# Optimization experiments

Measured on AMD Instinct MI355X. Metric: run time of the kernel, lower is better.

## Reference

```python
import jax, jax.numpy as jnp
import numpy as np

B, C, H, W = 8, 3, 512, 512
EPS = 2e-4
N_ITER = 10  # n_iter_max default in TvChambolleDenoiser.forward


def setup_inputs() -> dict:
    key = jax.random.key(0)
    k1, k2 = jax.random.split(key)
    image = jax.random.normal(k1, (B, C, H, W), dtype=jnp.float32)
    # per-image denoising strength, typical TV weights
    weight = jax.random.uniform(k2, (B,), dtype=jnp.float32, minval=0.05, maxval=0.15)
    return {"image": image, "weight": weight}


def _denoise_tv_2d(img, w, eps=EPS, n_iter=N_ITER):
    """Chambolle TV denoising of a single 2D image (faithful to the torch loop)."""
    tau = 0.25  # 1 / (2 * ndim), ndim = 2
    numel = img.shape[0] * img.shape[1]

    def body(carry, i):
        pt, out, E_init, E_prev, done = carry
        # divergence of dual variable pt: dt = -pt.sum(0); dt[1:,:] += pt[0,:-1,:]; dt[:,1:] += pt[1,:,:-1]
        dt = -(pt[0] + pt[1])
        dt = dt.at[1:, :].add(pt[0, :-1, :])
        dt = dt.at[:, 1:].add(pt[1, :, :-1])
        out_new = jnp.where(i > 0, img + dt, img)
        Et = jnp.where(i > 0, jnp.sum(dt * dt), jnp.float32(0.0))
        # forward finite differences, zero-padded at the far boundary (gt stays 0 there)
        g0 = jnp.pad(out_new[1:, :] - out_new[:-1, :], ((0, 1), (0, 0)))
        g1 = jnp.pad(out_new[:, 1:] - out_new[:, :-1], ((0, 0), (0, 1)))
        s = g0 * g0 + g1 * g1
        # safe sqrt (forward value identical; avoids NaN grads at exact zeros)
        norm = jnp.sqrt(jnp.where(s > 0, s, 1.0)) * (s > 0)
        Et = (Et + w * jnp.sum(norm)) / numel
        gt = jnp.stack([g0, g1])  # [2, H, W]
        pt_new = (pt - tau * gt) / (1.0 + (tau / w) * norm)[None]
        E_init_new = jnp.where(i == 0, Et, E_init)
        converged = (i > 0) & (jnp.abs(E_prev - Et) < eps * E_init_new)
        # once converged (break in the torch loop), freeze all state
        pt = jnp.where(done, pt, pt_new)
        out = jnp.where(done, out, out_new)
        E_prev = jnp.where(done, E_prev, Et)
        E_init = jnp.where(done, E_init, E_init_new)
        done = done | converged
        return (pt, out, E_init, E_prev, done), None

    carry0 = (
        jnp.zeros((2,) + img.shape, img.dtype),  # pt
        img,                                      # out
        jnp.float32(0.0),                         # E_init
        jnp.float32(0.0),                         # E_previous
        jnp.bool_(False),                         # done
    )
    (pt, out, E_init, E_prev, done), _ = jax.lax.scan(body, carry0, jnp.arange(n_iter))
    return out


def reference(image, weight):
    b, c, h, w = image.shape
    imgs = image.reshape(b * c, h, w)          # each (batch, channel) slice denoised independently
    ws = jnp.repeat(weight, c)                 # per-batch weight shared across channels
    out = jax.vmap(_denoise_tv_2d)(imgs, ws)
    return out.reshape(b, c, h, w)
```

## Files before the change

kernel.cpp:

```cpp
#include <hip/hip_runtime.h>
#include <hip/hip_fp16.h>
#include <math.h>
#include <stdint.h>

#define HH 512
#define WW 512
#define NIMG 24
#define CCH 3
#define TAU 0.25f
#define TVEPS 2e-4f
#define NUMEL 262144.0f

#define LSF 69
#define LSH 70


__device__ __forceinline__ float2 h2f(uint32_t v) {
    __half2 h; *reinterpret_cast<uint32_t*>(&h) = v;
    return __half22float2(h);
}
__device__ __forceinline__ uint32_t f2h2(float a, float b) {
    __half2 h = __floats2half2_rn(a, b);
    return *reinterpret_cast<uint32_t*>(&h);
}
__device__ __forceinline__ void h4_to_f(uint2 hv, float* f) {
    float2 a = h2f(hv.x), b = h2f(hv.y);
    f[0] = a.x; f[1] = a.y; f[2] = b.x; f[3] = b.y;
}

struct Smem {
    uint32_t PT[68 * LSF];
    float    OA[68 * LSF];
    __half   IM[68 * LSH];
};

__device__ __forceinline__ int SUMIX(int slot, int arr, int im) {
    return ((slot * 4 + arr) * NIMG + im) * 64;
}

__device__ void stage_pt_im(Smem& S, const uint32_t* __restrict__ ptg,
                            const __half* __restrict__ hI,
                            int x0, int y0, int tid) {
    for (int idx = tid; idx < 68 * 34; idx += 256) {
        int r = idx / 34, mq = idx - r * 34;
        int c = 2 * mq;
        int y = y0 - 2 + r, x = x0 - 2 + c;
        uint2 pv = make_uint2(0u, 0u);
        uint32_t iv = 0u;
        if ((unsigned)y < (unsigned)HH && (unsigned)x < (unsigned)WW) {
            size_t off = (size_t)y * WW + x;
            pv = *(const uint2*)(ptg + off);
            iv = *(const uint32_t*)(hI + off);
        }
        S.PT[r * LSF + c] = pv.x;
        S.PT[r * LSF + c + 1] = pv.y;
        *(uint32_t*)&S.IM[r * LSH + c] = iv;
    }
}

template <bool ACC>
__device__ float phase_outA(Smem& S, int tid) {
    float acc = 0.f;
    for (int idx = tid; idx < 67 * 67; idx += 256) {
        int r = idx / 67, c = idx - r * 67;
        r += 1; c += 1;
        float2 cf = h2f(S.PT[r * LSF + c]);
        float up = h2f(S.PT[(r - 1) * LSF + c]).x;
        float lf = h2f(S.PT[r * LSF + c - 1]).y;
        float im = __half2float(S.IM[r * LSH + c]);
        float oa = im + (-(cf.x + cf.y) + up + lf);
        S.OA[r * LSF + c] = oa;
        if (ACC) {
            if (r >= 2 && r < 66 && c >= 2 && c < 66) {
                float d = oa - im;
                acc += d * d;
            }
        }
    }
    return acc;
}

template <bool ACC>
__device__ float phase_ptA(Smem& S, int x0, int y0, int tid, float tw) {
    float acc = 0.f;
    for (int idx = tid; idx < 66 * 66; idx += 256) {
        int r = idx / 66, c = idx - r * 66;
        r += 1; c += 1;
        int y = y0 - 2 + r, x = x0 - 2 + c;
        if ((unsigned)y < (unsigned)HH && (unsigned)x < (unsigned)WW) {
            float o = S.OA[r * LSF + c];
            float g0 = (y < HH - 1) ? S.OA[(r + 1) * LSF + c] - o : 0.f;
            float g1 = (x < WW - 1) ? S.OA[r * LSF + c + 1] - o : 0.f;
            float ss2 = g0 * g0 + g1 * g1;
            float nrm = (ss2 > 0.f) ? sqrtf(ss2) : 0.f;
            if (ACC) {
                if (r >= 2 && r < 66 && c >= 2 && c < 66) acc += nrm;
            }
            float inv = __builtin_amdgcn_rcpf(1.f + tw * nrm);
            float2 cf = h2f(S.PT[r * LSF + c]);
            S.PT[r * LSF + c] = f2h2((cf.x - TAU * g0) * inv, (cf.y - TAU * g1) * inv);
        } else {
            S.PT[r * LSF + c] = 0u;
        }
    }
    return acc;
}

template <bool ACC>
__device__ float phase_outB(Smem& S, int tid) {
    float acc = 0.f;
    for (int idx = tid; idx < 65 * 65; idx += 256) {
        int r = idx / 65, c = idx - r * 65;
        r += 2; c += 2;
        float2 cf = h2f(S.PT[r * LSF + c]);
        float im = __half2float(S.IM[r * LSH + c]);
        float ob = im + (-(cf.x + cf.y) + h2f(S.PT[(r - 1) * LSF + c]).x
                         + h2f(S.PT[r * LSF + c - 1]).y);
        S.OA[r * LSF + c] = ob;
        if (ACC) {
            if (r < 66 && c < 66) {
                float d = ob - im;
                acc += d * d;
            }
        }
    }
    return acc;
}

__device__ float phase_ptB_store(Smem& S, uint32_t* __restrict__ poutI,
                                 int x0, int y0, int tid, float tw) {
    const int tx = tid & 15, ry = tid >> 4;
    const int gxb = x0 + 4 * tx;
    float acc = 0.f;
    #pragma unroll
    for (int i = 0; i < 4; ++i) {
        int gy = y0 + ry + 16 * i;
        int r = 2 + ry + 16 * i;
        uint32_t pv[4];
        #pragma unroll
        for (int j = 0; j < 4; ++j) {
            int c = 2 + 4 * tx + j;
            float o = S.OA[r * LSF + c];
            float g0 = (gy < HH - 1) ? S.OA[(r + 1) * LSF + c] - o : 0.f;
            float g1 = (gxb + j < WW - 1) ? S.OA[r * LSF + c + 1] - o : 0.f;
            float ss2 = g0 * g0 + g1 * g1;
            float nrm = (ss2 > 0.f) ? sqrtf(ss2) : 0.f;
            acc += nrm;
            float inv = __builtin_amdgcn_rcpf(1.f + tw * nrm);
            float2 cf = h2f(S.PT[r * LSF + c]);
            pv[j] = f2h2((cf.x - TAU * g0) * inv, (cf.y - TAU * g1) * inv);
        }
        *(uint4*)(poutI + (size_t)gy * WW + gxb) = make_uint4(pv[0], pv[1], pv[2], pv[3]);
    }
    return acc;
}

__device__ __forceinline__ void red4_store(float a, float b, float c, float d,
                                           float* pa, float* pb, float* pc, float* pdd,
                                           int tid) {
    for (int off = 32; off > 0; off >>= 1) {
        a += __shfl_down(a, off, 64);
        b += __shfl_down(b, off, 64);
        c += __shfl_down(c, off, 64);
        d += __shfl_down(d, off, 64);
    }
    __shared__ float sr[4][4];
    int wave = tid >> 6, lane = tid & 63;
    if (lane == 0) { sr[0][wave] = a; sr[1][wave] = b; sr[2][wave] = c; sr[3][wave] = d; }
    __syncthreads();
    if (tid == 0) {
        *pa = (sr[0][0] + sr[0][1]) + (sr[0][2] + sr[0][3]);
        *pb = (sr[1][0] + sr[1][1]) + (sr[1][2] + sr[1][3]);
        *pc = (sr[2][0] + sr[2][1]) + (sr[2][2] + sr[2][3]);
        *pdd = (sr[3][0] + sr[3][1]) + (sr[3][2] + sr[3][3]);
    }
}

__global__ __launch_bounds__(256, 4) void tv_step0(
    const float* __restrict__ img, const float* __restrict__ weight,
    __half* __restrict__ imgh, uint32_t* __restrict__ ptout,
    float* __restrict__ pn0)
{
    const int im = blockIdx.z;
    const int bid = blockIdx.y * 8 + blockIdx.x;
    const float w = weight[im / CCH];
    const int x0 = blockIdx.x * 64, y0 = blockIdx.y * 64;
    const float* imgI = img + (size_t)im * HH * WW;
    __half* hI = imgh + (size_t)im * HH * WW;
    uint32_t* pI = ptout + (size_t)im * HH * WW;
    __shared__ float s[65][68];
    const int tid = threadIdx.x;
    const int tx = tid & 15, ry = tid >> 4;
    const int gx = x0 + 4 * tx;

    float o[4][4];
    #pragma unroll
    for (int i = 0; i < 4; ++i) {
        int ey = ry + 16 * i, gy = y0 + ey;
        float4 v = *(const float4*)(imgI + (size_t)gy * WW + gx);
        o[i][0] = v.x; o[i][1] = v.y; o[i][2] = v.z; o[i][3] = v.w;
        *(float4*)&s[ey][4 * tx] = v;
    }
    if (tx == 15 && x0 + 64 < WW) {
        #pragma unroll
        for (int i = 0; i < 4; ++i) {
            int ey = ry + 16 * i, gy = y0 + ey;
            s[ey][64] = imgI[(size_t)gy * WW + x0 + 64];
        }
    }
    if (ry == 0 && y0 + 64 < HH) {
        *(float4*)&s[64][4 * tx] = *(const float4*)(imgI + (size_t)(y0 + 64) * WW + gx);
    }
    __syncthreads();

    float accn = 0.f;
    const float tw = TAU / w;
    #pragma unroll
    for (int i = 0; i < 4; ++i) {
        int ey = ry + 16 * i, gy = y0 + ey;
        float4 dn = *(float4*)&s[ey + 1][4 * tx];
        float rt_sh = __shfl_down(o[i][0], 1, 64);
        float rt = (tx == 15) ? s[ey][64] : rt_sh;
        float dnv[4] = {dn.x, dn.y, dn.z, dn.w};
        uint32_t pv[4];
        #pragma unroll
        for (int j = 0; j < 4; ++j) {
            float ov = o[i][j];
            float g0 = (gy < HH - 1) ? dnv[j] - ov : 0.f;
            float rn = (j < 3) ? o[i][j + 1] : rt;
            float g1 = (gx + j < WW - 1) ? rn - ov : 0.f;
            float ss2 = g0 * g0 + g1 * g1;
            float nrm = (ss2 > 0.f) ? sqrtf(ss2) : 0.f;
            accn += nrm;
            float inv = __builtin_amdgcn_rcpf(1.f + tw * nrm);
            pv[j] = f2h2(-TAU * g0 * inv, -TAU * g1 * inv);
        }
        size_t off = (size_t)gy * WW + gx;
        *(uint4*)(pI + off) = make_uint4(pv[0], pv[1], pv[2], pv[3]);
        *(uint2*)(hI + off) = make_uint2(f2h2(o[i][0], o[i][1]), f2h2(o[i][2], o[i][3]));
    }
    for (int off = 32; off > 0; off >>= 1) accn += __shfl_down(accn, off, 64);
    __shared__ float sr[4];
    if ((tid & 63) == 0) sr[tid >> 6] = accn;
    __syncthreads();
    if (tid == 0) pn0[im * 64 + bid] = (sr[0] + sr[1]) + (sr[2] + sr[3]);
}

__global__ __launch_bounds__(256, 3) void tv_fused(
    int m,
    const __half* __restrict__ imgh, const float* __restrict__ weight,
    const uint32_t* __restrict__ pt_in, uint32_t* __restrict__ pt_out,
    float* __restrict__ sc, float* __restrict__ sums)
{
    const int im = blockIdx.z;
    const int bid = blockIdx.y * 8 + blockIdx.x;
    const int tid = threadIdx.x;
    const float w = weight[im / CCH];

    __shared__ int sh_done;
    {
        const int sIn = (m - 1) & 1;
        if (tid < 64) {
            float da = 0.f, na = 0.f, db = 0.f, nb = 0.f;
            if (m == 1) {
                na = sums[SUMIX(0, 1, im) + tid];
            } else {
                da = sums[SUMIX(sIn, 0, im) + tid];
                na = sums[SUMIX(sIn, 1, im) + tid];
                db = sums[SUMIX(sIn, 2, im) + tid];
                nb = sums[SUMIX(sIn, 3, im) + tid];
            }
            for (int off = 32; off > 0; off >>= 1) {
                da += __shfl_down(da, off, 64);
                na += __shfl_down(na, off, 64);
                db += __shfl_down(db, off, 64);
                nb += __shfl_down(nb, off, 64);
            }
            if (tid == 0) {
                float Eprev, Einit; int done, lastk;
                if (m == 1) {
                    float E0 = w * na / NUMEL;
                    Eprev = E0; Einit = E0; done = 0; lastk = 0;
                } else {
                    const float* sI = sc + sIn * 128;
                    Eprev = sI[im]; Einit = sI[32 + im];
                    done = ((const int*)sI)[64 + im];
                    lastk = ((const int*)sI)[96 + im];
                    if (!done) {
                        float Et = (da + w * na) / NUMEL;
                        if (fabsf(Eprev - Et) < TVEPS * Einit) { done = 1; lastk = 2 * m - 3; }
                        else {
                            Eprev = Et;
                            Et = (db + w * nb) / NUMEL;
                            if (fabsf(Eprev - Et) < TVEPS * Einit) { done = 1; lastk = 2 * m - 2; }
                            else Eprev = Et;
                        }
                    }
                }
                if (bid == 0) {
                    float* sO = sc + (m & 1) * 128;
                    sO[im] = Eprev; sO[32 + im] = Einit;
                    ((int*)sO)[64 + im] = done;
                    ((int*)sO)[96 + im] = lastk;
                }
                sh_done = done;
            }
        }
    }
    __syncthreads();
    if (sh_done) return;

    const int x0 = blockIdx.x * 64, y0 = blockIdx.y * 64;
    const float tw = TAU / w;
    const uint32_t* pinI = pt_in + (size_t)im * HH * WW;
    uint32_t* poutI = pt_out + (size_t)im * HH * WW;
    const __half* hI = imgh + (size_t)im * HH * WW;

    __shared__ Smem S;
    stage_pt_im(S, pinI, hI, x0, y0, tid);
    __syncthreads();
    float a_d = phase_outA<true>(S, tid);
    __syncthreads();
    float a_n = phase_ptA<true>(S, x0, y0, tid, tw);
    __syncthreads();
    float b_d = phase_outB<true>(S, tid);
    __syncthreads();
    float b_n = phase_ptB_store(S, poutI, x0, y0, tid, tw);

    const int sOut = m & 1;
    red4_store(a_d, a_n, b_d, b_n,
               &sums[SUMIX(sOut, 0, im) + bid], &sums[SUMIX(sOut, 1, im) + bid],
               &sums[SUMIX(sOut, 2, im) + bid], &sums[SUMIX(sOut, 3, im) + bid], tid);
}

__global__ __launch_bounds__(256, 3) void tv_out(
    const float* __restrict__ img, float* __restrict__ out,
    const uint32_t* __restrict__ ptA, const uint32_t* __restrict__ ptB,
    const __half* __restrict__ imgh, const float* __restrict__ weight,
    const float* __restrict__ sc, const float* __restrict__ sums)
{
    const int im = blockIdx.z;
    const int tid = threadIdx.x;
    const float w = weight[im / CCH];

    __shared__ int2 shk;
    {
        const float* sI = sc;
        int done = ((const int*)sI)[64 + im];
        int lastk = ((const int*)sI)[96 + im];
        if (!done && tid < 64) {
            float da = sums[SUMIX(0, 0, im) + tid];
            float na = sums[SUMIX(0, 1, im) + tid];
            float db = sums[SUMIX(0, 2, im) + tid];
            float nb = sums[SUMIX(0, 3, im) + tid];
            for (int off = 32; off > 0; off >>= 1) {
                da += __shfl_down(da, off, 64);
                na += __shfl_down(na, off, 64);
                db += __shfl_down(db, off, 64);
                nb += __shfl_down(nb, off, 64);
            }
            if (tid == 0) {
                float Eprev = sI[im], Einit = sI[32 + im];
                float Et = (da + w * na) / NUMEL;
                if (fabsf(Eprev - Et) < TVEPS * Einit) { done = 1; lastk = 7; }
                else {
                    Eprev = Et;
                    Et = (db + w * nb) / NUMEL;
                    if (fabsf(Eprev - Et) < TVEPS * Einit) { done = 1; lastk = 8; }
                }
            }
        }
        if (tid == 0) { shk.x = done; shk.y = lastk; }
    }
    __syncthreads();
    const int k = shk.x ? shk.y : 9;

    const float* imgI = img + (size_t)im * HH * WW;
    float* outI = out + (size_t)im * HH * WW;
    const int x0 = blockIdx.x * 64, y0 = blockIdx.y * 64;
    const int tx = tid & 15, ry = tid >> 4;
    const int gx = x0 + 4 * tx;

    if (k & 1) {
        const uint32_t* p = ((((k - 1) >> 1) & 1) ? ptB : ptA) + (size_t)im * HH * WW;
        #pragma unroll
        for (int i = 0; i < 4; ++i) {
            int gy = y0 + ry + 16 * i;
            size_t off = (size_t)gy * WW + gx;
            uint4 cv = *(const uint4*)(p + off);
            uint4 uv = make_uint4(0u, 0u, 0u, 0u);
            if (gy > 0) uv = *(const uint4*)(p + off - WW);
            uint32_t lf = (gx > 0) ? p[off - 1] : 0u;
            float4 iv = *(const float4*)(imgI + off);
            uint32_t cc[4] = {cv.x, cv.y, cv.z, cv.w};
            uint32_t uu[4] = {uv.x, uv.y, uv.z, uv.w};
            uint32_t lt[4] = {lf, cv.x, cv.y, cv.z};
            float ivv[4] = {iv.x, iv.y, iv.z, iv.w};
            float r[4];
            #pragma unroll
            for (int j = 0; j < 4; ++j) {
                float2 cf = h2f(cc[j]);
                r[j] = ivv[j] + (-(cf.x + cf.y) + h2f(uu[j]).x + h2f(lt[j]).y);
            }
            *(float4*)(outI + off) = make_float4(r[0], r[1], r[2], r[3]);
        }
    } else {
        const uint32_t* p = ((((k - 2) >> 1) & 1) ? ptB : ptA) + (size_t)im * HH * WW;
        const __half* hI = imgh + (size_t)im * HH * WW;
        const float tw = TAU / w;
        __shared__ Smem S;
        stage_pt_im(S, p, hI, x0, y0, tid);
        __syncthreads();
        phase_outA<false>(S, tid);
        __syncthreads();
        phase_ptA<false>(S, x0, y0, tid, tw);
        __syncthreads();
        #pragma unroll
        for (int i = 0; i < 4; ++i) {
            int gy = y0 + ry + 16 * i;
            int r = 2 + ry + 16 * i;
            size_t off = (size_t)gy * WW + gx;
            float4 iv = *(const float4*)(imgI + off);
            float ivv[4] = {iv.x, iv.y, iv.z, iv.w};
            float rr[4];
            #pragma unroll
            for (int j = 0; j < 4; ++j) {
                int c = 2 + 4 * tx + j;
                float2 cf = h2f(S.PT[r * LSF + c]);
                float up = h2f(S.PT[(r - 1) * LSF + c]).x;
                float lf = h2f(S.PT[r * LSF + c - 1]).y;
                rr[j] = ivv[j] + (-(cf.x + cf.y) + up + lf);
            }
            *(float4*)(outI + off) = make_float4(rr[0], rr[1], rr[2], rr[3]);
        }
    }
}

extern "C" void kernel_launch(void* const* d_in, const int* in_sizes, int n_in,
                              void* d_out, int out_size, void* d_ws, size_t ws_size,
                              hipStream_t stream)
{
    const float* img = (const float*)d_in[0];
    const float* weight = (const float*)d_in[1];
    float* out = (float*)d_out;
    float* sc = (float*)d_ws;
    float* sums = (float*)((char*)d_ws + 4096);
    __half* imgh = (__half*)((char*)d_ws + 65536);
    uint32_t* ptA = (uint32_t*)((char*)d_ws + 12648448);
    uint32_t* ptB = (uint32_t*)((char*)d_ws + 37814272);

    dim3 grid(8, 8, NIMG);
    dim3 block(256);

    tv_step0<<<grid, block, 0, stream>>>(img, weight, imgh, ptA,
                                         sums + (0 * 4 + 1) * NIMG * 64);

    for (int m = 1; m <= 4; ++m) {
        uint32_t* pin  = (m & 1) ? ptA : ptB;
        uint32_t* pout = (m & 1) ? ptB : ptA;
        tv_fused<<<grid, block, 0, stream>>>(m, imgh, weight, pin, pout, sc, sums);
    }

    tv_out<<<grid, block, 0, stream>>>(img, out, ptA, ptB, imgh, weight, sc, sums);
}
```

Measured before the change: 280.2 us.

## Keep fused two-step TV tile in registers with shuffle-based halo exchange

The fused two-iteration kernel stops staging a 68x68 halo tile through shared memory with strided per-phase loops. Each thread now holds a 4x4 register patch, exchanges horizontal neighbours with wave shuffles and vertical neighbours through small shared buffers, and recomputes the one- and two-pixel halo ring explicitly on edge threads. This cuts LDS traffic and index arithmetic, at the cost of much higher register pressure (launch bounds lowered to 2 blocks per SIMD target) and more divergent edge-thread code.

```diff
diff --git a/kernel.cpp b/kernel.cpp
--- a/kernel.cpp
+++ b/kernel.cpp
@@ -28,15 +28,36 @@
     f[0] = a.x; f[1] = a.y; f[2] = b.x; f[3] = b.y;
 }
 
+__device__ __forceinline__ int SUMIX(int slot, int arr, int im) {
+    return ((slot * 4 + arr) * NIMG + im) * 64;
+}
+
+__device__ __forceinline__ void red4_store(float a, float b, float c, float d,
+                                           float* pa, float* pb, float* pc, float* pdd,
+                                           int tid) {
+    for (int off = 32; off > 0; off >>= 1) {
+        a += __shfl_down(a, off, 64);
+        b += __shfl_down(b, off, 64);
+        c += __shfl_down(c, off, 64);
+        d += __shfl_down(d, off, 64);
+    }
+    __shared__ float sr[4][4];
+    int wave = tid >> 6, lane = tid & 63;
+    if (lane == 0) { sr[0][wave] = a; sr[1][wave] = b; sr[2][wave] = c; sr[3][wave] = d; }
+    __syncthreads();
+    if (tid == 0) {
+        *pa = (sr[0][0] + sr[0][1]) + (sr[0][2] + sr[0][3]);
+        *pb = (sr[1][0] + sr[1][1]) + (sr[1][2] + sr[1][3]);
+        *pc = (sr[2][0] + sr[2][1]) + (sr[2][2] + sr[2][3]);
+        *pdd = (sr[3][0] + sr[3][1]) + (sr[3][2] + sr[3][3]);
+    }
+}
+
 struct Smem {
     uint32_t PT[68 * LSF];
     float    OA[68 * LSF];
     __half   IM[68 * LSH];
 };
-
-__device__ __forceinline__ int SUMIX(int slot, int arr, int im) {
-    return ((slot * 4 + arr) * NIMG + im) * 64;
-}
 
 __device__ void stage_pt_im(Smem& S, const uint32_t* __restrict__ ptg,
                             const __half* __restrict__ hI,
@@ -58,9 +79,7 @@
     }
 }
 
-template <bool ACC>
-__device__ float phase_outA(Smem& S, int tid) {
-    float acc = 0.f;
+__device__ void phase_outA_x(Smem& S, int tid) {
     for (int idx = tid; idx < 67 * 67; idx += 256) {
         int r = idx / 67, c = idx - r * 67;
         r += 1; c += 1;
@@ -68,21 +87,11 @@
         float up = h2f(S.PT[(r - 1) * LSF + c]).x;
         float lf = h2f(S.PT[r * LSF + c - 1]).y;
         float im = __half2float(S.IM[r * LSH + c]);
-        float oa = im + (-(cf.x + cf.y) + up + lf);
-        S.OA[r * LSF + c] = oa;
-        if (ACC) {
-            if (r >= 2 && r < 66 && c >= 2 && c < 66) {
-                float d = oa - im;
-                acc += d * d;
-            }
-        }
-    }
-    return acc;
-}
-
-template <bool ACC>
-__device__ float phase_ptA(Smem& S, int x0, int y0, int tid, float tw) {
-    float acc = 0.f;
+        S.OA[r * LSF + c] = im + (-(cf.x + cf.y) + up + lf);
+    }
+}
+
+__device__ void phase_ptA_x(Smem& S, int x0, int y0, int tid, float tw) {
     for (int idx = tid; idx < 66 * 66; idx += 256) {
         int r = idx / 66, c = idx - r * 66;
         r += 1; c += 1;
@@ -93,86 +102,12 @@
             float g1 = (x < WW - 1) ? S.OA[r * LSF + c + 1] - o : 0.f;
             float ss2 = g0 * g0 + g1 * g1;
             float nrm = (ss2 > 0.f) ? sqrtf(ss2) : 0.f;
-            if (ACC) {
-                if (r >= 2 && r < 66 && c >= 2 && c < 66) acc += nrm;
-            }
             float inv = __builtin_amdgcn_rcpf(1.f + tw * nrm);
             float2 cf = h2f(S.PT[r * LSF + c]);
             S.PT[r * LSF + c] = f2h2((cf.x - TAU * g0) * inv, (cf.y - TAU * g1) * inv);
         } else {
             S.PT[r * LSF + c] = 0u;
         }
-    }
-    return acc;
-}
-
-template <bool ACC>
-__device__ float phase_outB(Smem& S, int tid) {
-    float acc = 0.f;
-    for (int idx = tid; idx < 65 * 65; idx += 256) {
-        int r = idx / 65, c = idx - r * 65;
-        r += 2; c += 2;
-        float2 cf = h2f(S.PT[r * LSF + c]);
-        float im = __half2float(S.IM[r * LSH + c]);
-        float ob = im + (-(cf.x + cf.y) + h2f(S.PT[(r - 1) * LSF + c]).x
-                         + h2f(S.PT[r * LSF + c - 1]).y);
-        S.OA[r * LSF + c] = ob;
-        if (ACC) {
-            if (r < 66 && c < 66) {
-                float d = ob - im;
-                acc += d * d;
-            }
-        }
-    }
-    return acc;
-}
-
-__device__ float phase_ptB_store(Smem& S, uint32_t* __restrict__ poutI,
-                                 int x0, int y0, int tid, float tw) {
-    const int tx = tid & 15, ry = tid >> 4;
-    const int gxb = x0 + 4 * tx;
-    float acc = 0.f;
-    #pragma unroll
-    for (int i = 0; i < 4; ++i) {
-        int gy = y0 + ry + 16 * i;
-        int r = 2 + ry + 16 * i;
-        uint32_t pv[4];
-        #pragma unroll
-        for (int j = 0; j < 4; ++j) {
-            int c = 2 + 4 * tx + j;
-            float o = S.OA[r * LSF + c];
-            float g0 = (gy < HH - 1) ? S.OA[(r + 1) * LSF + c] - o : 0.f;
-            float g1 = (gxb + j < WW - 1) ? S.OA[r * LSF + c + 1] - o : 0.f;
-            float ss2 = g0 * g0 + g1 * g1;
-            float nrm = (ss2 > 0.f) ? sqrtf(ss2) : 0.f;
-            acc += nrm;
-            float inv = __builtin_amdgcn_rcpf(1.f + tw * nrm);
-            float2 cf = h2f(S.PT[r * LSF + c]);
-            pv[j] = f2h2((cf.x - TAU * g0) * inv, (cf.y - TAU * g1) * inv);
-        }
-        *(uint4*)(poutI + (size_t)gy * WW + gxb) = make_uint4(pv[0], pv[1], pv[2], pv[3]);
-    }
-    return acc;
-}
-
-__device__ __forceinline__ void red4_store(float a, float b, float c, float d,
-                                           float* pa, float* pb, float* pc, float* pdd,
-                                           int tid) {
-    for (int off = 32; off > 0; off >>= 1) {
-        a += __shfl_down(a, off, 64);
-        b += __shfl_down(b, off, 64);
-        c += __shfl_down(c, off, 64);
-        d += __shfl_down(d, off, 64);
-    }
-    __shared__ float sr[4][4];
-    int wave = tid >> 6, lane = tid & 63;
-    if (lane == 0) { sr[0][wave] = a; sr[1][wave] = b; sr[2][wave] = c; sr[3][wave] = d; }
-    __syncthreads();
-    if (tid == 0) {
-        *pa = (sr[0][0] + sr[0][1]) + (sr[0][2] + sr[0][3]);
-        *pb = (sr[1][0] + sr[1][1]) + (sr[1][2] + sr[1][3]);
-        *pc = (sr[2][0] + sr[2][1]) + (sr[2][2] + sr[2][3]);
-        *pdd = (sr[3][0] + sr[3][1]) + (sr[3][2] + sr[3][3]);
     }
 }
 
@@ -246,7 +181,7 @@
     if (tid == 0) pn0[im * 64 + bid] = (sr[0] + sr[1]) + (sr[2] + sr[3]);
 }
 
-__global__ __launch_bounds__(256, 3) void tv_fused(
+__global__ __launch_bounds__(256, 2) void tv_fused(
     int m,
     const __half* __restrict__ imgh, const float* __restrict__ weight,
     const uint32_t* __restrict__ pt_in, uint32_t* __restrict__ pt_out,
@@ -316,19 +251,419 @@
     uint32_t* poutI = pt_out + (size_t)im * HH * WW;
     const __half* hI = imgh + (size_t)im * HH * WW;
 
-    __shared__ Smem S;
-    stage_pt_im(S, pinI, hI, x0, y0, tid);
+    const int tx = tid & 15, ty = tid >> 4;
+    const int gx = x0 + 4 * tx, gy0 = y0 + 4 * ty;
+    const bool hasN = y0 > 0, hasW = x0 > 0;
+    const bool hasS = y0 + 64 < HH, hasE = x0 + 64 < WW;
+
+    __shared__ uint4  XB[16][16];
+    __shared__ float4 OB[16][16];
+    __shared__ float  WO[17];
+    __shared__ float  EO[17];
+    __shared__ uint32_t EP[16];
+
+    uint4 c[4]; uint2 ih[4];
+    #pragma unroll
+    for (int i = 0; i < 4; ++i) {
+        size_t off = (size_t)(gy0 + i) * WW + gx;
+        c[i] = *(const uint4*)(pinI + off);
+        ih[i] = *(const uint2*)(hI + off);
+    }
+    XB[ty][tx] = c[3];
+
+    uint4 png0 = make_uint4(0u,0u,0u,0u), png1 = make_uint4(0u,0u,0u,0u);
+    uint2 ihN = make_uint2(0u, 0u);
+    if (ty == 0 && hasN) {
+        png0 = *(const uint4*)(pinI + (size_t)(y0 - 2) * WW + gx);
+        png1 = *(const uint4*)(pinI + (size_t)(y0 - 1) * WW + gx);
+        ihN  = *(const uint2*)(hI + (size_t)(y0 - 1) * WW + gx);
+    }
+    uint32_t wp1[4] = {0u,0u,0u,0u}, wp2[4] = {0u,0u,0u,0u}, wup = 0u;
+    float ihW[4] = {0.f,0.f,0.f,0.f};
+    uint32_t wnp1 = 0u;
+    if (tx == 0 && hasW) {
+        #pragma unroll
+        for (int i = 0; i < 4; ++i) {
+            wp1[i] = pinI[(size_t)(gy0 + i) * WW + x0 - 1];
+            wp2[i] = pinI[(size_t)(gy0 + i) * WW + x0 - 2];
+            ihW[i] = __half2float(hI[(size_t)(gy0 + i) * WW + x0 - 1]);
+        }
+        if (gy0 > 0) wup = pinI[(size_t)(gy0 - 1) * WW + x0 - 1];
+        if (ty == 0 && hasN) wnp1 = pinI[(size_t)(y0 - 1) * WW + x0 - 1];
+    }
+    uint32_t ep1[4] = {0u,0u,0u,0u}, ep2[4] = {0u,0u,0u,0u}, epu1 = 0u, epu2 = 0u;
+    float ihE1[4] = {0.f,0.f,0.f,0.f}, ihE2[4] = {0.f,0.f,0.f,0.f};
+    uint32_t nep1 = 0u, nep2 = 0u, nepu1 = 0u, nepu2 = 0u;
+    float ihNE1 = 0.f, ihNE2 = 0.f;
+    if (tx == 15 && hasE) {
+        const int xe = x0 + 64;
+        #pragma unroll
+        for (int i = 0; i < 4; ++i) {
+            ep1[i] = pinI[(size_t)(gy0 + i) * WW + xe];
+            ep2[i] = pinI[(size_t)(gy0 + i) * WW + xe + 1];
+            ihE1[i] = __half2float(hI[(size_t)(gy0 + i) * WW + xe]);
+            ihE2[i] = __half2float(hI[(size_t)(gy0 + i) * WW + xe + 1]);
+        }
+        if (gy0 > 0) {
+            epu1 = pinI[(size_t)(gy0 - 1) * WW + xe];
+            epu2 = pinI[(size_t)(gy0 - 1) * WW + xe + 1];
+        }
+        if (ty == 0 && hasN) {
+            nep1 = pinI[(size_t)(y0 - 1) * WW + xe];
+            nep2 = pinI[(size_t)(y0 - 1) * WW + xe + 1];
+            nepu1 = pinI[(size_t)(y0 - 2) * WW + xe];
+            nepu2 = pinI[(size_t)(y0 - 2) * WW + xe + 1];
+            ihNE1 = __half2float(hI[(size_t)(y0 - 1) * WW + xe]);
+            ihNE2 = __half2float(hI[(size_t)(y0 - 1) * WW + xe + 1]);
+        }
+    }
+    uint4 sp1 = make_uint4(0u,0u,0u,0u), sp2 = make_uint4(0u,0u,0u,0u);
+    uint2 ihS1 = make_uint2(0u,0u), ihS2 = make_uint2(0u,0u);
+    uint32_t wsp1 = 0u, wsp2 = 0u, wsl1 = 0u, wsl2 = 0u;
+    float ihSW1 = 0.f, ihSW2 = 0.f;
+    uint32_t sep = 0u; float ihSE = 0.f;
+    if (ty == 15 && hasS) {
+        sp1 = *(const uint4*)(pinI + (size_t)(y0 + 64) * WW + gx);
+        sp2 = *(const uint4*)(pinI + (size_t)(y0 + 65) * WW + gx);
+        ihS1 = *(const uint2*)(hI + (size_t)(y0 + 64) * WW + gx);
+        ihS2 = *(const uint2*)(hI + (size_t)(y0 + 65) * WW + gx);
+        if (tx == 0 && hasW) {
+            wsp1 = pinI[(size_t)(y0 + 64) * WW + x0 - 1];
+            wsp2 = pinI[(size_t)(y0 + 65) * WW + x0 - 1];
+            wsl1 = pinI[(size_t)(y0 + 64) * WW + x0 - 2];
+            wsl2 = pinI[(size_t)(y0 + 65) * WW + x0 - 2];
+            ihSW1 = __half2float(hI[(size_t)(y0 + 64) * WW + x0 - 1]);
+            ihSW2 = __half2float(hI[(size_t)(y0 + 65) * WW + x0 - 1]);
+        }
+        if (tx == 15 && hasE) {
+            sep = pinI[(size_t)(y0 + 64) * WW + x0 + 64];
+            ihSE = __half2float(hI[(size_t)(y0 + 64) * WW + x0 + 64]);
+        }
+    }
     __syncthreads();
-    float a_d = phase_outA<true>(S, tid);
+
+    float o[4][4];
+    float accda = 0.f;
+    {
+        uint4 up4 = (ty > 0) ? XB[ty - 1][tx] : png1;
+        uint32_t ua[4] = {up4.x, up4.y, up4.z, up4.w};
+        #pragma unroll
+        for (int i = 0; i < 4; ++i) {
+            uint32_t ca[4] = {c[i].x, c[i].y, c[i].z, c[i].w};
+            uint32_t pr[4] = {c[i].x, c[i].y, c[i].z, c[i].w};
+            uint32_t lsh = __shfl_up(c[i].w, 1, 64);
+            uint32_t lw = (tx > 0) ? lsh : wp1[i];
+            uint32_t cu[4] = {(i > 0) ? (&c[i-1].x)[0] : ua[0],
+                              (i > 0) ? (&c[i-1].x)[1] : ua[1],
+                              (i > 0) ? (&c[i-1].x)[2] : ua[2],
+                              (i > 0) ? (&c[i-1].x)[3] : ua[3]};
+            float imv[4]; h4_to_f(ih[i], imv);
+            #pragma unroll
+            for (int j = 0; j < 4; ++j) {
+                float2 cf = h2f(ca[j]);
+                float up = h2f(cu[j]).x;
+                float le = (j > 0) ? h2f(pr[j - 1]).y : h2f(lw).y;
+                float dv = -(cf.x + cf.y) + up + le;
+                o[i][j] = imv[j] + dv;
+                accda += dv * dv;
+            }
+        }
+    }
+    float oN[4] = {0.f,0.f,0.f,0.f};
+    if (ty == 0) {
+        uint32_t pga[4] = {png1.x, png1.y, png1.z, png1.w};
+        uint32_t p0a[4] = {png0.x, png0.y, png0.z, png0.w};
+        uint32_t nsh = __shfl_up(png1.w, 1, 64);
+        uint32_t nlw = (tx > 0) ? nsh : wnp1;
+        float imn[4]; h4_to_f(ihN, imn);
+        #pragma unroll
+        for (int j = 0; j < 4; ++j) {
+            float2 cf = h2f(pga[j]);
+            float up = h2f(p0a[j]).x;
+            float le = (j > 0) ? h2f(pga[j - 1]).y : h2f(nlw).y;
+            oN[j] = imn[j] + (-(cf.x + cf.y) + up + le);
+        }
+    }
+    float oW[4] = {0.f,0.f,0.f,0.f};
+    if (tx == 0) {
+        #pragma unroll
+        for (int i = 0; i < 4; ++i) {
+            float2 cf = h2f(wp1[i]);
+            float up = (i > 0) ? h2f(wp1[i - 1]).x : h2f(wup).x;
+            float le = h2f(wp2[i]).y;
+            oW[i] = ihW[i] + (-(cf.x + cf.y) + up + le);
+        }
+    }
+    float oE1[4] = {0.f,0.f,0.f,0.f}, oE2[4] = {0.f,0.f,0.f,0.f};
+    if (tx == 15) {
+        #pragma unroll
+        for (int i = 0; i < 4; ++i) {
+            float2 cf = h2f(ep1[i]);
+            float up = (i > 0) ? h2f(ep1[i - 1]).x : h2f(epu1).x;
+            float le = h2f(c[i].w).y;
+            oE1[i] = ihE1[i] + (-(cf.x + cf.y) + up + le);
+            float2 cg = h2f(ep2[i]);
+            float up2 = (i > 0) ? h2f(ep2[i - 1]).x : h2f(epu2).x;
+            float le2 = h2f(ep1[i]).y;
+            oE2[i] = ihE2[i] + (-(cg.x + cg.y) + up2 + le2);
+        }
+    }
+    float oNE1 = 0.f, oNE2 = 0.f;
+    if (tx == 15 && ty == 0) {
+        float2 cf = h2f(nep1);
+        oNE1 = ihNE1 + (-(cf.x + cf.y) + h2f(nepu1).x + h2f(png1.w).y);
+        float2 cg = h2f(nep2);
+        oNE2 = ihNE2 + (-(cg.x + cg.y) + h2f(nepu2).x + h2f(nep1).y);
+    }
+    float oS1[4] = {0.f,0.f,0.f,0.f}, oS2[4] = {0.f,0.f,0.f,0.f};
+    if (ty == 15) {
+        uint32_t s1a[4] = {sp1.x, sp1.y, sp1.z, sp1.w};
+        uint32_t s2a[4] = {sp2.x, sp2.y, sp2.z, sp2.w};
+        uint32_t c3a[4] = {c[3].x, c[3].y, c[3].z, c[3].w};
+        uint32_t s1sh = __shfl_up(sp1.w, 1, 64);
+        uint32_t s2sh = __shfl_up(sp2.w, 1, 64);
+        uint32_t s1l = (tx > 0) ? s1sh : wsp1;
+        uint32_t s2l = (tx > 0) ? s2sh : wsp2;
+        float im1[4]; h4_to_f(ihS1, im1);
+        float im2[4]; h4_to_f(ihS2, im2);
+        #pragma unroll
+        for (int j = 0; j < 4; ++j) {
+            float2 cf = h2f(s1a[j]);
+            float up = h2f(c3a[j]).x;
+            float le = (j > 0) ? h2f(s1a[j - 1]).y : h2f(s1l).y;
+            oS1[j] = im1[j] + (-(cf.x + cf.y) + up + le);
+            float2 cg = h2f(s2a[j]);
+            float up2 = h2f(s1a[j]).x;
+            float le2 = (j > 0) ? h2f(s2a[j - 1]).y : h2f(s2l).y;
+            oS2[j] = im2[j] + (-(cg.x + cg.y) + up2 + le2);
+        }
+    }
+    float oSW1 = 0.f, oSW2 = 0.f;
+    if (tx == 0 && ty == 15) {
+        float2 cf = h2f(wsp1);
+        oSW1 = ihSW1 + (-(cf.x + cf.y) + h2f(wp1[3]).x + h2f(wsl1).y);
+        float2 cg = h2f(wsp2);
+        oSW2 = ihSW2 + (-(cg.x + cg.y) + h2f(wsp1).x + h2f(wsl2).y);
+    }
+    float oSE = 0.f;
+    if (tx == 15 && ty == 15) {
+        float2 cf = h2f(sep);
+        oSE = ihSE + (-(cf.x + cf.y) + h2f(ep1[3]).x + h2f(sp1.w).y);
+    }
+
+    OB[ty][tx] = make_float4(o[0][0], o[0][1], o[0][2], o[0][3]);
+    if (tx == 0) WO[ty] = oW[0];
+    if (tx == 0 && ty == 15) WO[16] = oSW1;
+    if (tx == 15) EO[ty] = oE1[0];
+    if (tx == 15 && ty == 15) EO[16] = oSE;
     __syncthreads();
-    float a_n = phase_ptA<true>(S, x0, y0, tid, tw);
+
+    uint32_t pa[4][4];
+    float accna = 0.f;
+    {
+        float bel4[4];
+        if (ty < 15) {
+            float4 t = OB[ty + 1][tx];
+            bel4[0] = t.x; bel4[1] = t.y; bel4[2] = t.z; bel4[3] = t.w;
+        } else {
+            bel4[0] = oS1[0]; bel4[1] = oS1[1]; bel4[2] = oS1[2]; bel4[3] = oS1[3];
+        }
+        #pragma unroll
+        for (int i = 0; i < 4; ++i) {
+            int gy = gy0 + i;
+            float rsh = __shfl_down(o[i][0], 1, 64);
+            float rt = (tx < 15) ? rsh : oE1[i];
+            uint32_t ca[4] = {c[i].x, c[i].y, c[i].z, c[i].w};
+            #pragma unroll
+            for (int j = 0; j < 4; ++j) {
+                float ov = o[i][j];
+                float bel = (i < 3) ? o[i + 1][j] : bel4[j];
+                float g0 = (gy < HH - 1) ? bel - ov : 0.f;
+                float rn = (j < 3) ? o[i][j + 1] : rt;
+                float g1 = (gx + j < WW - 1) ? rn - ov : 0.f;
+                float ss2 = g0 * g0 + g1 * g1;
+                float nrm = (ss2 > 0.f) ? sqrtf(ss2) : 0.f;
+                accna += nrm;
+                float inv = __builtin_amdgcn_rcpf(1.f + tw * nrm);
+                float2 cf = h2f(ca[j]);
+                pa[i][j] = f2h2((cf.x - TAU * g0) * inv, (cf.y - TAU * g1) * inv);
+            }
+        }
+    }
+    uint32_t paN[4] = {0u,0u,0u,0u};
+    if (ty == 0 && hasN) {
+        uint32_t pga[4] = {png1.x, png1.y, png1.z, png1.w};
+        float rsh = __shfl_down(oN[0], 1, 64);
+        #pragma unroll
+        for (int j = 0; j < 4; ++j) {
+            float ov = oN[j];
+            float g0 = o[0][j] - ov;
+            float rn = (j < 3) ? oN[j + 1] : ((tx < 15) ? rsh : oNE1);
+            float g1 = (gx + j < WW - 1) ? rn - ov : 0.f;
+            float ss2 = g0 * g0 + g1 * g1;
+            float nrm = (ss2 > 0.f) ? sqrtf(ss2) : 0.f;
+            float inv = __builtin_amdgcn_rcpf(1.f + tw * nrm);
+            float2 cf = h2f(pga[j]);
+            paN[j] = f2h2((cf.x - TAU * g0) * inv, (cf.y - TAU * g1) * inv);
+        }
+    }
+    uint32_t paW[4] = {0u,0u,0u,0u};
+    if (tx == 0 && hasW) {
+        #pragma unroll
+        for (int i = 0; i < 4; ++i) {
+            int gy = gy0 + i;
+            float ov = oW[i];
+            float bel = (i < 3) ? oW[i + 1] : WO[ty + 1];
+            float g0 = (gy < HH - 1) ? bel - ov : 0.f;
+            float g1 = o[i][0] - ov;
+            float ss2 = g0 * g0 + g1 * g1;
+            float nrm = (ss2 > 0.f) ? sqrtf(ss2) : 0.f;
+            float inv = __builtin_amdgcn_rcpf(1.f + tw * nrm);
+            float2 cf = h2f(wp1[i]);
+            paW[i] = f2h2((cf.x - TAU * g0) * inv, (cf.y - TAU * g1) * inv);
+        }
+    }
+    uint32_t paS[4] = {0u,0u,0u,0u};
+    if (ty == 15 && hasS) {
+        uint32_t s1a[4] = {sp1.x, sp1.y, sp1.z, sp1.w};
+        float rsh = __shfl_down(oS1[0], 1, 64);
+        #pragma unroll
+        for (int j = 0; j < 4; ++j) {
+            float ov = oS1[j];
+            float g0 = oS2[j] - ov;
+            float rn = (j < 3) ? oS1[j + 1] : ((tx < 15) ? rsh : oSE);
+            float g1 = (gx + j < WW - 1) ? rn - ov : 0.f;
+            float ss2 = g0 * g0 + g1 * g1;
+            float nrm = (ss2 > 0.f) ? sqrtf(ss2) : 0.f;
+            float inv = __builtin_amdgcn_rcpf(1.f + tw * nrm);
+            float2 cf = h2f(s1a[j]);
+            paS[j] = f2h2((cf.x - TAU * g0) * inv, (cf.y - TAU * g1) * inv);
+        }
+    }
+    uint32_t paE[4] = {0u,0u,0u,0u};
+    if (tx == 15 && hasE) {
+        #pragma unroll
+        for (int i = 0; i < 4; ++i) {
+            int gy = gy0 + i;
+            float ov = oE1[i];
+            float bel = (i < 3) ? oE1[i + 1] : EO[ty + 1];
+            float g0 = (gy < HH - 1) ? bel - ov : 0.f;
+            float g1 = oE2[i] - ov;
+            float ss2 = g0 * g0 + g1 * g1;
+            float nrm = (ss2 > 0.f) ? sqrtf(ss2) : 0.f;
+            float inv = __builtin_amdgcn_rcpf(1.f + tw * nrm);
+            float2 cf = h2f(ep1[i]);
+            paE[i] = f2h2((cf.x - TAU * g0) * inv, (cf.y - TAU * g1) * inv);
+        }
+    }
+    uint32_t paNE = 0u;
+    if (tx == 15 && ty == 0 && hasN && hasE) {
+        float ov = oNE1;
+        float g0 = oE1[0] - ov;
+        float g1 = oNE2 - ov;
+        float ss2 = g0 * g0 + g1 * g1;
+        float nrm = (ss2 > 0.f) ? sqrtf(ss2) : 0.f;
+        float inv = __builtin_amdgcn_rcpf(1.f + tw * nrm);
+        float2 cf = h2f(nep1);
+        paNE = f2h2((cf.x - TAU * g0) * inv, (cf.y - TAU * g1) * inv);
+    }
+    uint32_t paSW = 0u;
+    if (tx == 0 && ty == 15 && hasS && hasW) {
+        float ov = oSW1;
+        float g0 = oSW2 - ov;
+        float g1 = oS1[0] - ov;
+        float ss2 = g0 * g0 + g1 * g1;
+        float nrm = (ss2 > 0.f) ? sqrtf(ss2) : 0.f;
+        float inv = __builtin_amdgcn_rcpf(1.f + tw * nrm);
+        float2 cf = h2f(wsp1);
+        paSW = f2h2((cf.x - TAU * g0) * inv, (cf.y - TAU * g1) * inv);
+    }
+    XB[ty][tx] = make_uint4(pa[3][0], pa[3][1], pa[3][2], pa[3][3]);
+    if (tx == 15) EP[ty] = paE[3];
     __syncthreads();
-    float b_d = phase_outB<true>(S, tid);
+
+    float ob[4][4];
+    float accdb = 0.f;
+    {
+        uint4 up4 = (ty > 0) ? XB[ty - 1][tx] : make_uint4(paN[0], paN[1], paN[2], paN[3]);
+        uint32_t ua[4] = {up4.x, up4.y, up4.z, up4.w};
+        #pragma unroll
+        for (int i = 0; i < 4; ++i) {
+            uint32_t lsh = __shfl_up(pa[i][3], 1, 64);
+            uint32_t lw = (tx > 0) ? lsh : paW[i];
+            float imv[4]; h4_to_f(ih[i], imv);
+            #pragma unroll
+            for (int j = 0; j < 4; ++j) {
+                float2 cf = h2f(pa[i][j]);
+                float up = (i > 0) ? h2f(pa[i - 1][j]).x : h2f(ua[j]).x;
+                float le = (j > 0) ? h2f(pa[i][j - 1]).y : h2f(lw).y;
+                float dv = -(cf.x + cf.y) + up + le;
+                ob[i][j] = imv[j] + dv;
+                accdb += dv * dv;
+            }
+        }
+    }
+    float obS[4] = {0.f,0.f,0.f,0.f};
+    if (ty == 15 && hasS) {
+        uint32_t ssh = __shfl_up(paS[3], 1, 64);
+        uint32_t sl = (tx > 0) ? ssh : paSW;
+        float im1[4]; h4_to_f(ihS1, im1);
+        #pragma unroll
+        for (int j = 0; j < 4; ++j) {
+            float2 cf = h2f(paS[j]);
+            float up = h2f(pa[3][j]).x;
+            float le = (j > 0) ? h2f(paS[j - 1]).y : h2f(sl).y;
+            obS[j] = im1[j] + (-(cf.x + cf.y) + up + le);
+        }
+    }
+    float obE[4] = {0.f,0.f,0.f,0.f};
+    if (tx == 15 && hasE) {
+        #pragma unroll
+        for (int i = 0; i < 4; ++i) {
+            float2 cf = h2f(paE[i]);
+            float up = (i > 0) ? h2f(paE[i - 1]).x
+                               : ((ty > 0) ? h2f(EP[ty - 1]).x : h2f(paNE).x);
+            float le = h2f(pa[i][3]).y;
+            obE[i] = ihE1[i] + (-(cf.x + cf.y) + up + le);
+        }
+    }
+    OB[ty][tx] = make_float4(ob[0][0], ob[0][1], ob[0][2], ob[0][3]);
     __syncthreads();
-    float b_n = phase_ptB_store(S, poutI, x0, y0, tid, tw);
-
+
+    float accnb = 0.f;
+    {
+        float bel4[4];
+        if (ty < 15) {
+            float4 t = OB[ty + 1][tx];
+            bel4[0] = t.x; bel4[1] = t.y; bel4[2] = t.z; bel4[3] = t.w;
+        } else {
+            bel4[0] = obS[0]; bel4[1] = obS[1]; bel4[2] = obS[2]; bel4[3] = obS[3];
+        }
+        #pragma unroll
+        for (int i = 0; i < 4; ++i) {
+            int gy = gy0 + i;
+            float rsh = __shfl_down(ob[i][0], 1, 64);
+            float rt = (tx < 15) ? rsh : obE[i];
+            uint32_t pv[4];
+            #pragma unroll
+            for (int j = 0; j < 4; ++j) {
+                float ov = ob[i][j];
+                float bel = (i < 3) ? ob[i + 1][j] : bel4[j];
+                float g0 = (gy < HH - 1) ? bel - ov : 0.f;
+                float rn = (j < 3) ? ob[i][j + 1] : rt;
+                float g1 = (gx + j < WW - 1) ? rn - ov : 0.f;
+                float ss2 = g0 * g0 + g1 * g1;
+                float nrm = (ss2 > 0.f) ? sqrtf(ss2) : 0.f;
+                accnb += nrm;
+                float inv = __builtin_amdgcn_rcpf(1.f + tw * nrm);
+                float2 cf = h2f(pa[i][j]);
+                pv[j] = f2h2((cf.x - TAU * g0) * inv, (cf.y - TAU * g1) * inv);
+            }
+            *(uint4*)(poutI + (size_t)gy * WW + gx) = make_uint4(pv[0], pv[1], pv[2], pv[3]);
+        }
+    }
     const int sOut = m & 1;
-    red4_store(a_d, a_n, b_d, b_n,
+    red4_store(accda, accna, accdb, accnb,
                &sums[SUMIX(sOut, 0, im) + bid], &sums[SUMIX(sOut, 1, im) + bid],
                &sums[SUMIX(sOut, 2, im) + bid], &sums[SUMIX(sOut, 3, im) + bid], tid);
 }
@@ -411,9 +746,9 @@
         __shared__ Smem S;
         stage_pt_im(S, p, hI, x0, y0, tid);
         __syncthreads();
-        phase_outA<false>(S, tid);
+        phase_outA_x(S, tid);
         __syncthreads();
-        phase_ptA<false>(S, x0, y0, tid, tw);
+        phase_ptA_x(S, x0, y0, tid, tw);
         __syncthreads();
         #pragma unroll
         for (int i = 0; i < 4; ++i) {
@@ -425,10 +760,10 @@
             float rr[4];
             #pragma unroll
             for (int j = 0; j < 4; ++j) {
-                int c = 2 + 4 * tx + j;
-                float2 cf = h2f(S.PT[r * LSF + c]);
-                float up = h2f(S.PT[(r - 1) * LSF + c]).x;
-                float lf = h2f(S.PT[r * LSF + c - 1]).y;
+                int cix = 2 + 4 * tx + j;
+                float2 cf = h2f(S.PT[r * LSF + cix]);
+                float up = h2f(S.PT[(r - 1) * LSF + cix]).x;
+                float lf = h2f(S.PT[r * LSF + cix - 1]).y;
                 rr[j] = ivv[j] + (-(cf.x + cf.y) + up + lf);
             }
             *(float4*)(outI + off) = make_float4(rr[0], rr[1], rr[2], rr[3]);
```

Result: faster. 236.2 us (-15.7%).
